# Performance work log

Hardware: AMD Instinct MI355X
Metric: run time of the kernel (lower is better)

The kernel has to match this reference:

```python
import jax, jax.numpy as jnp
import numpy as np

N = 10000
E = 160000
F_IN = 64
HID = 128
HEADS = 8
NC = 3
NEG_SLOPE = 0.2
EPS = 1e-16


def setup_inputs() -> dict:
    key = jax.random.key(0)
    ks = jax.random.split(key, 12)
    p = lambda k, shape: jax.random.normal(k, shape, jnp.float32) * 0.1
    return {
        "x": jax.random.normal(ks[0], (N, F_IN), jnp.float32),
        "edge_index": jax.random.randint(ks[1], (2, E), 0, N),
        # conv1: F_IN -> 8 heads x 128, concat -> 1024
        "W1": p(ks[2], (F_IN, HEADS * HID)),
        "a_src1": p(ks[3], (HEADS, HID)),
        "a_dst1": p(ks[4], (HEADS, HID)),
        "b1": jnp.zeros((HEADS * HID,), jnp.float32),
        # conv2: 1024 -> 8 heads x 64, concat -> 512
        "W2": p(ks[5], (HEADS * HID, HEADS * (HID // 2))),
        "a_src2": p(ks[6], (HEADS, HID // 2)),
        "a_dst2": p(ks[7], (HEADS, HID // 2)),
        "b2": jnp.zeros((HEADS * (HID // 2),), jnp.float32),
        # conv3: 512 -> 1 head x 3, mean (concat=False)
        "W3": p(ks[8], (HEADS * (HID // 2), NC)),
        "a_src3": p(ks[9], (1, NC)),
        "a_dst3": p(ks[10], (1, NC)),
        "b3": jnp.zeros((NC,), jnp.float32),
    }


def gat_conv(x, src, dst, W, a_src, a_dst, b, concat):
    """PyG-style GATConv (eval mode, self-loops already in src/dst)."""
    n = x.shape[0]
    H, C = a_src.shape
    h = (x @ W).reshape(n, H, C)                      # [N, H, C]
    s_src = jnp.sum(h * a_src[None], axis=-1)         # [N, H]
    s_dst = jnp.sum(h * a_dst[None], axis=-1)         # [N, H]
    e = jax.nn.leaky_relu(s_src[src] + s_dst[dst], NEG_SLOPE)  # [E, H]
    # segment softmax over incoming edges per destination node
    m = jax.ops.segment_max(e, dst, num_segments=n)   # [N, H]
    ex = jnp.exp(e - m[dst])
    denom = jax.ops.segment_sum(ex, dst, num_segments=n)
    alpha = ex / (denom[dst] + EPS)                   # [E, H]
    msg = h[src] * alpha[:, :, None]                  # [E, H, C]
    out = jax.ops.segment_sum(msg, dst, num_segments=n)  # [N, H, C]
    out = out.reshape(n, H * C) if concat else out.mean(axis=1)
    return out + b


def reference(x, edge_index, W1, a_src1, a_dst1, b1, W2, a_src2, a_dst2, b2, W3, a_src3, a_dst3, b3):
    n = x.shape[0]
    loop = jnp.arange(n, dtype=edge_index.dtype)
    src = jnp.concatenate([edge_index[0], loop])
    dst = jnp.concatenate([edge_index[1], loop])
    h = gat_conv(x, src, dst, W1, a_src1, a_dst1, b1, True)
    h = jax.nn.elu(h)
    h = gat_conv(h, src, dst, W2, a_src2, a_dst2, b2, True)
    h = jax.nn.elu(h)
    h = gat_conv(h, src, dst, W3, a_src3, a_dst3, b3, False)
    return jax.nn.log_softmax(h, axis=1)
```

## Files before the change

kernel.cpp:

```cpp
#include <hip/hip_runtime.h>
#include <math.h>

#define NEG_SLOPE 0.2f
#define EPS_DEN 1e-16f

typedef __attribute__((ext_vector_type(8))) short bf16x8;
typedef __attribute__((ext_vector_type(4))) float f32x4;

__device__ inline void split2(float a, short& hi, short& lo) {
    unsigned u = __float_as_uint(a);
    unsigned uh = (u + 0x8000u) & 0xFFFF0000u;
    float fh = __uint_as_float(uh);
    hi = (short)(uh >> 16);
    float r = a - fh;
    lo = (short)((__float_as_uint(r) + 0x8000u) >> 16);
}

__device__ inline unsigned short f2bf(float f) {
    unsigned u = __float_as_uint(f);
    return (unsigned short)((u + 0x7FFFu + ((u >> 16) & 1u)) >> 16);
}
__device__ inline float bflo(unsigned u) { return __uint_as_float(u << 16); }
__device__ inline float bfhi(unsigned u) { return __uint_as_float(u & 0xFFFF0000u); }

__global__ void k_count(const int* __restrict__ ei, int E, int Nn, int* counts) {
    int e = blockIdx.x * blockDim.x + threadIdx.x;
    int ET = E + Nn;
    if (e >= ET) return;
    int d = (e < E) ? ei[E + e] : (e - E);
    atomicAdd(&counts[d], 1);
}

__global__ void k_scan(const int* __restrict__ counts, int Nn, int ET, int* __restrict__ row_off) {
    __shared__ int lds[256];
    int t = threadIdx.x;
    int chunk = (Nn + 255) / 256;
    int b0 = t * chunk, b1 = min(Nn, b0 + chunk);
    int s = 0;
    for (int i = b0; i < b1; i++) s += counts[i];
    lds[t] = s;
    __syncthreads();
    #pragma unroll
    for (int d = 1; d < 256; d <<= 1) {
        int v = (t >= d) ? lds[t - d] : 0;
        __syncthreads();
        lds[t] += v;
        __syncthreads();
    }
    int run = (t == 0) ? 0 : lds[t - 1];
    for (int i = b0; i < b1; i++) { row_off[i] = run; run += counts[i]; }
    if (t == 0) row_off[Nn] = ET;
}

__global__ void k_scatter(const int* __restrict__ ei, int E, int Nn,
                          const int* __restrict__ row_off, int* cursor, int* __restrict__ col) {
    int e = blockIdx.x * blockDim.x + threadIdx.x;
    int ET = E + Nn;
    if (e >= ET) return;
    int d = (e < E) ? ei[E + e] : (e - E);
    int s = (e < E) ? ei[e] : (e - E);
    int pos = atomicAdd(&cursor[d], 1);
    col[row_off[d] + pos] = s;
}

__global__ void k_split_x(const float* __restrict__ x, short* __restrict__ A,
                          int M, int Mp, int K) {
    int i = blockIdx.x * blockDim.x + threadIdx.x;
    if (i >= Mp * K) return;
    int row = i / K, c = i - row * K;
    float v = (row < M) ? x[(size_t)row * K + c] : 0.f;
    short hi, lo;
    split2(v, hi, lo);
    A[(size_t)row * (2 * K) + c] = hi;
    A[(size_t)row * (2 * K) + K + c] = lo;
}

__global__ __launch_bounds__(256) void k_split_wt(const float* __restrict__ W,
                                                  short* __restrict__ Bt, int K, int N, int dup) {
    __shared__ float s[32][33];
    int k0 = blockIdx.x * 32, n0 = blockIdx.y * 32;
    int tx = threadIdx.x & 31, ty = threadIdx.x >> 5;
    for (int r = ty; r < 32; r += 8) s[r][tx] = W[(size_t)(k0 + r) * N + n0 + tx];
    __syncthreads();
    int ldbt = (1 + dup) * K;
    for (int r = ty; r < 32; r += 8) {
        float v = s[tx][r];
        unsigned u = __float_as_uint(v);
        short hi = (short)((u + 0x7FFFu + ((u >> 16) & 1u)) >> 16);
        size_t base = (size_t)(n0 + r) * ldbt + k0 + tx;
        Bt[base] = hi;
        if (dup) Bt[base + K] = hi;
    }
}

template<bool FUSESC>
__global__ __launch_bounds__(256) void k_mfma64(const short* __restrict__ A,
                                                const short* __restrict__ B,
                                                unsigned short* __restrict__ C,
                                                const float* __restrict__ a_src,
                                                const float* __restrict__ a_dst,
                                                float* __restrict__ ssrc,
                                                float* __restrict__ sdst,
                                                int M, int N, int Ktot,
                                                int lda, int ldb) {
    __shared__ short As[64 * 32];
    __shared__ short Bs[64 * 32];
    __shared__ float sred[4][64][2];
    int t = threadIdx.x;
    int lane = t & 63;
    int wid = t >> 6;

    int nbx = N >> 6;
    int nb = gridDim.x;
    int q = nb >> 3, r = nb & 7;
    int xcd = blockIdx.x & 7, pos = blockIdx.x >> 3;
    int L = (xcd < r ? xcd * (q + 1) : r * (q + 1) + (xcd - r) * q) + pos;
    int bn = (L % nbx) * 64;
    int bm = (L / nbx) * 64;

    int wm = (wid >> 1) * 32, wn = (wid & 1) * 32;
    int fr = lane & 15, kq = lane >> 4;

    int srow = t >> 2, sslot = t & 3;
    int sko = ((sslot ^ ((srow >> 1) & 3)) << 3);

    f32x4 acc[2][2] = {};

    for (int k0 = 0; k0 < Ktot; k0 += 32) {
        {
            const short* sa = A + (size_t)(bm + srow) * lda + k0 + sko;
            const short* sb = B + (size_t)(bn + srow) * ldb + k0 + sko;
            short* da = As + (size_t)(wid << 6) * 8;
            short* db = Bs + (size_t)(wid << 6) * 8;
            __builtin_amdgcn_global_load_lds((const __attribute__((address_space(1))) void*)sa,
                                             (__attribute__((address_space(3))) void*)da, 16, 0, 0);
            __builtin_amdgcn_global_load_lds((const __attribute__((address_space(1))) void*)sb,
                                             (__attribute__((address_space(3))) void*)db, 16, 0, 0);
        }
        __syncthreads();
        bf16x8 af[2], bfv[2];
        #pragma unroll
        for (int i = 0; i < 2; i++) {
            int rowa = wm + i * 16 + fr;
            int rowb = wn + i * 16 + fr;
            af[i]  = *(const bf16x8*)(As + rowa * 32 + ((kq ^ ((rowa >> 1) & 3)) << 3));
            bfv[i] = *(const bf16x8*)(Bs + rowb * 32 + ((kq ^ ((rowb >> 1) & 3)) << 3));
        }
        #pragma unroll
        for (int i = 0; i < 2; i++)
            #pragma unroll
            for (int j = 0; j < 2; j++)
                acc[i][j] = __builtin_amdgcn_mfma_f32_16x16x32_bf16(af[i], bfv[j], acc[i][j], 0, 0, 0);
        __syncthreads();
    }
    #pragma unroll
    for (int i = 0; i < 2; i++) {
        int rbase = bm + wm + i * 16 + kq * 4;
        #pragma unroll
        for (int j = 0; j < 2; j++) {
            int colc = bn + wn + j * 16 + fr;
            #pragma unroll
            for (int rg = 0; rg < 4; rg++) {
                int rr = rbase + rg;
                if (rr < M) C[(size_t)rr * N + colc] = f2bf(acc[i][j][rg]);
            }
        }
    }
    if (FUSESC) {
        float asv[2], adv[2];
        #pragma unroll
        for (int j = 0; j < 2; j++) {
            int colc = bn + wn + j * 16 + fr;
            asv[j] = a_src[colc];
            adv[j] = a_dst[colc];
        }
        float ps[8], pd[8];
        #pragma unroll
        for (int i = 0; i < 2; i++)
            #pragma unroll
            for (int rg = 0; rg < 4; rg++) {
                int k8 = i * 4 + rg;
                ps[k8] = acc[i][0][rg] * asv[0] + acc[i][1][rg] * asv[1];
                pd[k8] = acc[i][0][rg] * adv[0] + acc[i][1][rg] * adv[1];
            }
        #pragma unroll
        for (int k8 = 0; k8 < 8; k8++) {
            #pragma unroll
            for (int off = 1; off < 16; off <<= 1) {
                ps[k8] += __shfl_xor(ps[k8], off);
                pd[k8] += __shfl_xor(pd[k8], off);
            }
        }
        if (fr == 0) {
            #pragma unroll
            for (int i = 0; i < 2; i++)
                #pragma unroll
                for (int rg = 0; rg < 4; rg++) {
                    int rl = wm + i * 16 + kq * 4 + rg;
                    sred[wid][rl][0] = ps[i * 4 + rg];
                    sred[wid][rl][1] = pd[i * 4 + rg];
                }
        }
        __syncthreads();
        if ((wid & 1) == 0 && fr == 0) {
            int hh = bn >> 6;
            #pragma unroll
            for (int i = 0; i < 2; i++)
                #pragma unroll
                for (int rg = 0; rg < 4; rg++) {
                    int rl = wm + i * 16 + kq * 4 + rg;
                    int rr = bm + rl;
                    if (rr < M) {
                        ssrc[rr * 8 + hh] = sred[wid][rl][0] + sred[wid | 1][rl][0];
                        sdst[rr * 8 + hh] = sred[wid][rl][1] + sred[wid | 1][rl][1];
                    }
                }
        }
    }
}

template<int H, int C>
__global__ __launch_bounds__(256) void k_scores_bf(const unsigned short* __restrict__ h,
                                                   const float* __restrict__ a_src,
                                                   const float* __restrict__ a_dst,
                                                   float* __restrict__ ssrc,
                                                   float* __restrict__ sdst, int Nn) {
    constexpr int D = H * C;
    constexpr int PER = D / 64;
    constexpr int GRP = C / PER;
    int lane = threadIdx.x & 63;
    int n = blockIdx.x * 4 + (threadIdx.x >> 6);
    if (n >= Nn) return;
    const unsigned short* hp = h + (size_t)n * D + lane * PER;
    int cb = lane * PER;
    float as = 0.f, ad = 0.f;
    #pragma unroll
    for (int j0 = 0; j0 < PER; j0 += 8) {
        uint4 u = *(const uint4*)(hp + j0);
        int c = cb + j0;
        as += bflo(u.x) * a_src[c + 0] + bfhi(u.x) * a_src[c + 1]
            + bflo(u.y) * a_src[c + 2] + bfhi(u.y) * a_src[c + 3]
            + bflo(u.z) * a_src[c + 4] + bfhi(u.z) * a_src[c + 5]
            + bflo(u.w) * a_src[c + 6] + bfhi(u.w) * a_src[c + 7];
        ad += bflo(u.x) * a_dst[c + 0] + bfhi(u.x) * a_dst[c + 1]
            + bflo(u.y) * a_dst[c + 2] + bfhi(u.y) * a_dst[c + 3]
            + bflo(u.z) * a_dst[c + 4] + bfhi(u.z) * a_dst[c + 5]
            + bflo(u.w) * a_dst[c + 6] + bfhi(u.w) * a_dst[c + 7];
    }
    #pragma unroll
    for (int off = GRP >> 1; off >= 1; off >>= 1) {
        as += __shfl_xor(as, off);
        ad += __shfl_xor(ad, off);
    }
    if ((lane & (GRP - 1)) == 0) {
        int hh = lane / GRP;
        ssrc[n * H + hh] = as;
        sdst[n * H + hh] = ad;
    }
}

template<int H, int C, int CB, bool ELU, bool BFOUT>
__global__ __launch_bounds__(256) void k_agg_wave(const unsigned short* __restrict__ hsrc,
                                                  const float* __restrict__ ssrc,
                                                  const float* __restrict__ sdst,
                                                  const int* __restrict__ col,
                                                  const int* __restrict__ row_off,
                                                  const float* __restrict__ bias,
                                                  float* __restrict__ out,
                                                  unsigned short* __restrict__ osp,
                                                  int nw) {
    constexpr int D = H * C;
    int lane = threadIdx.x & 63;
    int w = blockIdx.x * 4 + (threadIdx.x >> 6);
    if (w >= nw) return;
    int n, cb;
    if (CB == 2) { n = w >> 1; cb = w & 1; } else { n = w; cb = 0; }
    int col0 = cb * 512 + lane * 8;
    int myhead = col0 / C;
    float sd = sdst[n * H + myhead];
    int beg = row_off[n], end = row_off[n + 1];
    const unsigned short* hbase = hsrc + col0;

    float acc[8] = {0.f, 0.f, 0.f, 0.f, 0.f, 0.f, 0.f, 0.f};
    float den = 0.f;
    #pragma unroll 2
    for (int j = beg; j < end; j++) {
        int cj = col[j];
        float s = ssrc[cj * H + myhead] + sd;
        s = (s >= 0.f) ? s : NEG_SLOPE * s;
        float ex = __expf(s);
        den += ex;
        uint4 u = *(const uint4*)(hbase + (size_t)cj * D);
        acc[0] += ex * bflo(u.x); acc[1] += ex * bfhi(u.x);
        acc[2] += ex * bflo(u.y); acc[3] += ex * bfhi(u.y);
        acc[4] += ex * bflo(u.z); acc[5] += ex * bfhi(u.z);
        acc[6] += ex * bflo(u.w); acc[7] += ex * bfhi(u.w);
    }
    float iv = 1.f / (den + EPS_DEN);
    float vals[8];
    #pragma unroll
    for (int v = 0; v < 8; v++) {
        float val = acc[v] * iv + bias[col0 + v];
        if (ELU) val = (val > 0.f) ? val : (__expf(val) - 1.f);
        vals[v] = val;
    }
    if (BFOUT) {
        uint4 o;
        o.x = (unsigned)f2bf(vals[0]) | ((unsigned)f2bf(vals[1]) << 16);
        o.y = (unsigned)f2bf(vals[2]) | ((unsigned)f2bf(vals[3]) << 16);
        o.z = (unsigned)f2bf(vals[4]) | ((unsigned)f2bf(vals[5]) << 16);
        o.w = (unsigned)f2bf(vals[6]) | ((unsigned)f2bf(vals[7]) << 16);
        *(uint4*)(osp + (size_t)n * D + col0) = o;
    } else {
        *(f32x4*)(out + (size_t)n * D + col0) = *(f32x4*)&vals[0];
        *(f32x4*)(out + (size_t)n * D + col0 + 4) = *(f32x4*)&vals[4];
    }
}

__global__ __launch_bounds__(256) void k_agg2_l3(const unsigned short* __restrict__ hsrc,
                                                 const float* __restrict__ ssrc,
                                                 const float* __restrict__ sdst,
                                                 const int* __restrict__ col,
                                                 const int* __restrict__ row_off,
                                                 const float* __restrict__ bias,
                                                 const float* __restrict__ W3,
                                                 const float* __restrict__ as3,
                                                 const float* __restrict__ ad3,
                                                 float* __restrict__ h3,
                                                 float* __restrict__ ssrc3,
                                                 float* __restrict__ sdst3,
                                                 int Nn) {
    constexpr int D = 512;
    int lane = threadIdx.x & 63;
    int n = blockIdx.x * 4 + (threadIdx.x >> 6);
    if (n >= Nn) return;
    int col0 = lane * 8;
    int myhead = lane >> 3;
    float sd = sdst[n * 8 + myhead];
    int beg = row_off[n], end = row_off[n + 1];
    const unsigned short* hbase = hsrc + col0;

    float acc[8] = {0.f, 0.f, 0.f, 0.f, 0.f, 0.f, 0.f, 0.f};
    float den = 0.f;
    #pragma unroll 2
    for (int j = beg; j < end; j++) {
        int cj = col[j];
        float s = ssrc[cj * 8 + myhead] + sd;
        s = (s >= 0.f) ? s : NEG_SLOPE * s;
        float ex = __expf(s);
        den += ex;
        uint4 u = *(const uint4*)(hbase + (size_t)cj * D);
        acc[0] += ex * bflo(u.x); acc[1] += ex * bfhi(u.x);
        acc[2] += ex * bflo(u.y); acc[3] += ex * bfhi(u.y);
        acc[4] += ex * bflo(u.z); acc[5] += ex * bfhi(u.z);
        acc[6] += ex * bflo(u.w); acc[7] += ex * bfhi(u.w);
    }
    float iv = 1.f / (den + EPS_DEN);
    float t0 = 0.f, t1 = 0.f, t2 = 0.f;
    #pragma unroll
    for (int v = 0; v < 8; v++) {
        float val = acc[v] * iv + bias[col0 + v];
        val = (val > 0.f) ? val : (__expf(val) - 1.f);
        const float* wp = W3 + (size_t)(col0 + v) * 3;
        t0 += val * wp[0];
        t1 += val * wp[1];
        t2 += val * wp[2];
    }
    #pragma unroll
    for (int off = 32; off >= 1; off >>= 1) {
        t0 += __shfl_xor(t0, off);
        t1 += __shfl_xor(t1, off);
        t2 += __shfl_xor(t2, off);
    }
    if (lane == 0) {
        h3[n * 3 + 0] = t0; h3[n * 3 + 1] = t1; h3[n * 3 + 2] = t2;
        ssrc3[n] = t0 * as3[0] + t1 * as3[1] + t2 * as3[2];
        sdst3[n] = t0 * ad3[0] + t1 * ad3[1] + t2 * ad3[2];
    }
}

__global__ void k_l3_fused(const float* __restrict__ h3, const float* __restrict__ ssrc,
                           const float* __restrict__ sdst, const int* __restrict__ col,
                           const int* __restrict__ row_off, const float* __restrict__ b3,
                           float* __restrict__ out, int Nn) {
    int n = blockIdx.x * blockDim.x + threadIdx.x;
    if (n >= Nn) return;
    int beg = row_off[n], end = row_off[n + 1];
    float sd = sdst[n];
    float den = 0.f, a0 = 0.f, a1 = 0.f, a2 = 0.f;
    for (int j = beg; j < end; j++) {
        int sI = col[j];
        float s = ssrc[sI] + sd;
        s = (s >= 0.f) ? s : NEG_SLOPE * s;
        float ex = __expf(s);
        den += ex;
        a0 += ex * h3[sI * 3 + 0];
        a1 += ex * h3[sI * 3 + 1];
        a2 += ex * h3[sI * 3 + 2];
    }
    float iv = 1.f / (den + EPS_DEN);
    float v0 = a0 * iv + b3[0], v1 = a1 * iv + b3[1], v2 = a2 * iv + b3[2];
    float m = fmaxf(v0, fmaxf(v1, v2));
    float l = logf(__expf(v0 - m) + __expf(v1 - m) + __expf(v2 - m));
    out[n * 3 + 0] = v0 - m - l;
    out[n * 3 + 1] = v1 - m - l;
    out[n * 3 + 2] = v2 - m - l;
}

extern "C" void kernel_launch(void* const* d_in, const int* in_sizes, int n_in,
                              void* d_out, int out_size, void* d_ws, size_t ws_size,
                              hipStream_t stream) {
    (void)n_in; (void)out_size; (void)ws_size;
    const float* x   = (const float*)d_in[0];
    const int*   ei  = (const int*)d_in[1];
    const float* W1  = (const float*)d_in[2];
    const float* as1 = (const float*)d_in[3];
    const float* ad1 = (const float*)d_in[4];
    const float* b1  = (const float*)d_in[5];
    const float* W2  = (const float*)d_in[6];
    const float* as2 = (const float*)d_in[7];
    const float* ad2 = (const float*)d_in[8];
    const float* b2  = (const float*)d_in[9];
    const float* W3  = (const float*)d_in[10];
    const float* as3 = (const float*)d_in[11];
    const float* ad3 = (const float*)d_in[12];
    const float* b3  = (const float*)d_in[13];
    float* out = (float*)d_out;

    const int Nn = in_sizes[0] / 64;
    const int E  = in_sizes[1] / 2;
    const int ET = E + Nn;
    const int Mp = ((Nn + 127) / 128) * 128;

    char* ws = (char*)d_ws;
    size_t off = 0;
    auto alloc = [&](size_t bytes) -> void* {
        void* p = ws + off;
        off = (off + bytes + 255) & ~(size_t)255;
        return p;
    };
    unsigned short* hbuf = (unsigned short*)alloc((size_t)Mp * 1024 * 2);
    unsigned short* A2   = (unsigned short*)alloc((size_t)Mp * 1024 * 2);
    float* h3   = (float*)alloc((size_t)Nn * 3 * 4);
    short* A1   = (short*)alloc((size_t)Mp * 128 * 2);
    short* B1t  = (short*)alloc((size_t)1024 * 128 * 2);
    short* B2t  = (short*)alloc((size_t)512 * 1024 * 2);
    float* ssrc = (float*)alloc((size_t)Nn * 8 * 4);
    float* sdst = (float*)alloc((size_t)Nn * 8 * 4);
    float* ssrcB= (float*)alloc((size_t)Nn * 8 * 4);
    float* sdstB= (float*)alloc((size_t)Nn * 8 * 4);
    float* ssrc3= (float*)alloc((size_t)Nn * 4);
    float* sdst3= (float*)alloc((size_t)Nn * 4);
    int* counts = (int*)alloc((size_t)Nn * 2 * 4);
    int* cursor = counts + Nn;
    int* row_off= (int*)alloc((size_t)(Nn + 1) * 4);
    int* colb   = (int*)alloc((size_t)ET * 4);

    hipMemsetAsync(counts, 0, (size_t)Nn * 2 * 4, stream);

    int etb = (ET + 255) / 256;
    k_count<<<etb, 256, 0, stream>>>(ei, E, Nn, counts);
    k_scan<<<1, 256, 0, stream>>>(counts, Nn, ET, row_off);
    k_scatter<<<etb, 256, 0, stream>>>(ei, E, Nn, row_off, cursor, colb);

    k_split_x<<<(Mp * 64 + 255) / 256, 256, 0, stream>>>(x, A1, Nn, Mp, 64);
    k_split_wt<<<dim3(64 / 32, 1024 / 32), 256, 0, stream>>>(W1, B1t, 64, 1024, 1);
    k_split_wt<<<dim3(1024 / 32, 512 / 32), 256, 0, stream>>>(W2, B2t, 1024, 512, 0);

    {
        int nb = (1024 / 64) * (Mp / 64);
        k_mfma64<false><<<nb, 256, 0, stream>>>(A1, B1t, hbuf, nullptr, nullptr, nullptr, nullptr,
                                                Nn, 1024, 128, 128, 128);
        k_scores_bf<8, 128><<<(Nn + 3) / 4, 256, 0, stream>>>(hbuf, as1, ad1, ssrc, sdst, Nn);
        int nw = Nn * 2;
        k_agg_wave<8, 128, 2, true, true><<<(nw + 3) / 4, 256, 0, stream>>>(
            hbuf, ssrc, sdst, colb, row_off, b1, nullptr, A2, nw);
    }
    {
        int nb = (512 / 64) * (Mp / 64);
        k_mfma64<true><<<nb, 256, 0, stream>>>((const short*)A2, B2t, hbuf, as2, ad2, ssrcB, sdstB,
                                               Nn, 512, 1024, 1024, 1024);
        k_agg2_l3<<<(Nn + 3) / 4, 256, 0, stream>>>(hbuf, ssrcB, sdstB, colb, row_off, b2,
                                                    W3, as3, ad3, h3, ssrc3, sdst3, Nn);
    }
    k_l3_fused<<<(Nn + 255) / 256, 256, 0, stream>>>(h3, ssrc3, sdst3, colb, row_off, b3, out, Nn);
}
```

Before: 190.3 us.

## Merge preprocessing kernels and fuse layer-1 attention scores into a wider GEMM

The separate count, x-split and two weight-split kernels are folded into one k_pre launch that routes blocks to each task by block index. For layer 1, a new GEMM kernel with 64x128 tiles covers one full head per block and computes the src/dst attention scores in its epilogue, so the standalone k_scores_bf pass that re-read the 1024-wide bf16 hidden buffer is removed. This saves several launches and one full read of the layer-1 features, at the cost of more accumulator registers in the wider tile and a more complex block-routing kernel.

Measured after the change: 182.3 us. -4.2%, faster.

```diff
diff --git a/kernel.cpp b/kernel.cpp
--- a/kernel.cpp
+++ b/kernel.cpp
@@ -23,63 +23,50 @@
 __device__ inline float bflo(unsigned u) { return __uint_as_float(u << 16); }
 __device__ inline float bfhi(unsigned u) { return __uint_as_float(u & 0xFFFF0000u); }
 
-__global__ void k_count(const int* __restrict__ ei, int E, int Nn, int* counts) {
-    int e = blockIdx.x * blockDim.x + threadIdx.x;
+__global__ __launch_bounds__(256) void k_pre(const int* __restrict__ ei, int E, int Nn,
+                                             int* __restrict__ counts,
+                                             const float* __restrict__ x, short* __restrict__ A1, int Mp,
+                                             const float* __restrict__ W1, short* __restrict__ B1t,
+                                             const float* __restrict__ W2, short* __restrict__ B2t) {
+    __shared__ float s[32][33];
+    int t = threadIdx.x;
+    int b = blockIdx.x;
     int ET = E + Nn;
-    if (e >= ET) return;
-    int d = (e < E) ? ei[E + e] : (e - E);
-    atomicAdd(&counts[d], 1);
-}
-
-__global__ void k_scan(const int* __restrict__ counts, int Nn, int ET, int* __restrict__ row_off) {
-    __shared__ int lds[256];
-    int t = threadIdx.x;
-    int chunk = (Nn + 255) / 256;
-    int b0 = t * chunk, b1 = min(Nn, b0 + chunk);
-    int s = 0;
-    for (int i = b0; i < b1; i++) s += counts[i];
-    lds[t] = s;
-    __syncthreads();
-    #pragma unroll
-    for (int d = 1; d < 256; d <<= 1) {
-        int v = (t >= d) ? lds[t - d] : 0;
-        __syncthreads();
-        lds[t] += v;
-        __syncthreads();
-    }
-    int run = (t == 0) ? 0 : lds[t - 1];
-    for (int i = b0; i < b1; i++) { row_off[i] = run; run += counts[i]; }
-    if (t == 0) row_off[Nn] = ET;
-}
-
-__global__ void k_scatter(const int* __restrict__ ei, int E, int Nn,
-                          const int* __restrict__ row_off, int* cursor, int* __restrict__ col) {
-    int e = blockIdx.x * blockDim.x + threadIdx.x;
-    int ET = E + Nn;
-    if (e >= ET) return;
-    int d = (e < E) ? ei[E + e] : (e - E);
-    int s = (e < E) ? ei[e] : (e - E);
-    int pos = atomicAdd(&cursor[d], 1);
-    col[row_off[d] + pos] = s;
-}
-
-__global__ void k_split_x(const float* __restrict__ x, short* __restrict__ A,
-                          int M, int Mp, int K) {
-    int i = blockIdx.x * blockDim.x + threadIdx.x;
-    if (i >= Mp * K) return;
-    int row = i / K, c = i - row * K;
-    float v = (row < M) ? x[(size_t)row * K + c] : 0.f;
-    short hi, lo;
-    split2(v, hi, lo);
-    A[(size_t)row * (2 * K) + c] = hi;
-    A[(size_t)row * (2 * K) + K + c] = lo;
-}
-
-__global__ __launch_bounds__(256) void k_split_wt(const float* __restrict__ W,
-                                                  short* __restrict__ Bt, int K, int N, int dup) {
-    __shared__ float s[32][33];
-    int k0 = blockIdx.x * 32, n0 = blockIdx.y * 32;
-    int tx = threadIdx.x & 31, ty = threadIdx.x >> 5;
+    int etb = (ET + 255) / 256;
+    int xb = (Mp * 64 + 255) / 256;
+    if (b < etb) {
+        int e = b * 256 + t;
+        if (e < ET) {
+            int d = (e < E) ? ei[E + e] : (e - E);
+            atomicAdd(&counts[d], 1);
+        }
+        return;
+    }
+    b -= etb;
+    if (b < xb) {
+        int i = b * 256 + t;
+        if (i < Mp * 64) {
+            int row = i >> 6, c = i & 63;
+            float v = (row < Nn) ? x[(size_t)row * 64 + c] : 0.f;
+            short hi, lo;
+            split2(v, hi, lo);
+            A1[(size_t)row * 128 + c] = hi;
+            A1[(size_t)row * 128 + 64 + c] = lo;
+        }
+        return;
+    }
+    b -= xb;
+    const float* W; short* Bt; int K, N, dup, kb, nb;
+    if (b < 64) {
+        W = W1; Bt = B1t; K = 64; N = 1024; dup = 1;
+        kb = b & 1; nb = b >> 1;
+    } else {
+        b -= 64;
+        W = W2; Bt = B2t; K = 1024; N = 512; dup = 0;
+        kb = b & 31; nb = b >> 5;
+    }
+    int k0 = kb * 32, n0 = nb * 32;
+    int tx = t & 31, ty = t >> 5;
     for (int r = ty; r < 32; r += 8) s[r][tx] = W[(size_t)(k0 + r) * N + n0 + tx];
     __syncthreads();
     int ldbt = (1 + dup) * K;
@@ -93,7 +80,172 @@
     }
 }
 
-template<bool FUSESC>
+__global__ void k_scan(const int* __restrict__ counts, int Nn, int ET, int* __restrict__ row_off) {
+    __shared__ int lds[256];
+    int t = threadIdx.x;
+    int chunk = (Nn + 255) / 256;
+    int b0 = t * chunk, b1 = min(Nn, b0 + chunk);
+    int s = 0;
+    for (int i = b0; i < b1; i++) s += counts[i];
+    lds[t] = s;
+    __syncthreads();
+    #pragma unroll
+    for (int d = 1; d < 256; d <<= 1) {
+        int v = (t >= d) ? lds[t - d] : 0;
+        __syncthreads();
+        lds[t] += v;
+        __syncthreads();
+    }
+    int run = (t == 0) ? 0 : lds[t - 1];
+    for (int i = b0; i < b1; i++) { row_off[i] = run; run += counts[i]; }
+    if (t == 0) row_off[Nn] = ET;
+}
+
+__global__ void k_scatter(const int* __restrict__ ei, int E, int Nn,
+                          const int* __restrict__ row_off, int* cursor, int* __restrict__ col) {
+    int e = blockIdx.x * blockDim.x + threadIdx.x;
+    int ET = E + Nn;
+    if (e >= ET) return;
+    int d = (e < E) ? ei[E + e] : (e - E);
+    int s = (e < E) ? ei[e] : (e - E);
+    int pos = atomicAdd(&cursor[d], 1);
+    col[row_off[d] + pos] = s;
+}
+
+__global__ __launch_bounds__(256) void k_mfma_w(const short* __restrict__ A,
+                                                const short* __restrict__ B,
+                                                unsigned short* __restrict__ C,
+                                                const float* __restrict__ a_src,
+                                                const float* __restrict__ a_dst,
+                                                float* __restrict__ ssrc,
+                                                float* __restrict__ sdst,
+                                                int M, int N, int Ktot,
+                                                int lda, int ldb) {
+    __shared__ short As[64 * 32];
+    __shared__ short Bs[128 * 32];
+    __shared__ float sred[4][64][2];
+    int t = threadIdx.x;
+    int lane = t & 63;
+    int wid = t >> 6;
+
+    int nbx = N >> 7;
+    int nb = gridDim.x;
+    int q = nb >> 3, r = nb & 7;
+    int xcd = blockIdx.x & 7, pos = blockIdx.x >> 3;
+    int L = (xcd < r ? xcd * (q + 1) : r * (q + 1) + (xcd - r) * q) + pos;
+    int bn = (L % nbx) * 128;
+    int bm = (L / nbx) * 64;
+
+    int wm = (wid & 1) * 32, wn = (wid >> 1) * 64;
+    int fr = lane & 15, kq = lane >> 4;
+
+    int srow = t >> 2, sslot = t & 3;
+    int sko = ((sslot ^ ((srow >> 1) & 3)) << 3);
+
+    f32x4 acc[2][4] = {};
+
+    for (int k0 = 0; k0 < Ktot; k0 += 32) {
+        {
+            const short* sa = A + (size_t)(bm + srow) * lda + k0 + sko;
+            short* da = As + (size_t)(wid << 6) * 8;
+            __builtin_amdgcn_global_load_lds((const __attribute__((address_space(1))) void*)sa,
+                                             (__attribute__((address_space(3))) void*)da, 16, 0, 0);
+            #pragma unroll
+            for (int qq = 0; qq < 2; qq++) {
+                int v = qq * 256 + t;
+                int rowb = v >> 2, slotb = v & 3;
+                int skob = ((slotb ^ ((rowb >> 1) & 3)) << 3);
+                const short* sb = B + (size_t)(bn + rowb) * ldb + k0 + skob;
+                short* db = Bs + (size_t)(qq * 256 + (wid << 6)) * 8;
+                __builtin_amdgcn_global_load_lds((const __attribute__((address_space(1))) void*)sb,
+                                                 (__attribute__((address_space(3))) void*)db, 16, 0, 0);
+            }
+        }
+        __syncthreads();
+        bf16x8 af[2], bfv[4];
+        #pragma unroll
+        for (int i = 0; i < 2; i++) {
+            int rowa = wm + i * 16 + fr;
+            af[i] = *(const bf16x8*)(As + rowa * 32 + ((kq ^ ((rowa >> 1) & 3)) << 3));
+        }
+        #pragma unroll
+        for (int j = 0; j < 4; j++) {
+            int rowb = wn + j * 16 + fr;
+            bfv[j] = *(const bf16x8*)(Bs + rowb * 32 + ((kq ^ ((rowb >> 1) & 3)) << 3));
+        }
+        #pragma unroll
+        for (int i = 0; i < 2; i++)
+            #pragma unroll
+            for (int j = 0; j < 4; j++)
+                acc[i][j] = __builtin_amdgcn_mfma_f32_16x16x32_bf16(af[i], bfv[j], acc[i][j], 0, 0, 0);
+        __syncthreads();
+    }
+    #pragma unroll
+    for (int i = 0; i < 2; i++) {
+        int rbase = bm + wm + i * 16 + kq * 4;
+        #pragma unroll
+        for (int j = 0; j < 4; j++) {
+            int colc = bn + wn + j * 16 + fr;
+            #pragma unroll
+            for (int rg = 0; rg < 4; rg++) {
+                int rr = rbase + rg;
+                if (rr < M) C[(size_t)rr * N + colc] = f2bf(acc[i][j][rg]);
+            }
+        }
+    }
+    float asv[4], adv[4];
+    #pragma unroll
+    for (int j = 0; j < 4; j++) {
+        int colc = bn + wn + j * 16 + fr;
+        asv[j] = a_src[colc];
+        adv[j] = a_dst[colc];
+    }
+    float ps[8], pd[8];
+    #pragma unroll
+    for (int i = 0; i < 2; i++)
+        #pragma unroll
+        for (int rg = 0; rg < 4; rg++) {
+            int k8 = i * 4 + rg;
+            ps[k8] = acc[i][0][rg] * asv[0] + acc[i][1][rg] * asv[1]
+                   + acc[i][2][rg] * asv[2] + acc[i][3][rg] * asv[3];
+            pd[k8] = acc[i][0][rg] * adv[0] + acc[i][1][rg] * adv[1]
+                   + acc[i][2][rg] * adv[2] + acc[i][3][rg] * adv[3];
+        }
+    #pragma unroll
+    for (int k8 = 0; k8 < 8; k8++) {
+        #pragma unroll
+        for (int off = 1; off < 16; off <<= 1) {
+            ps[k8] += __shfl_xor(ps[k8], off);
+            pd[k8] += __shfl_xor(pd[k8], off);
+        }
+    }
+    if (fr == 0) {
+        #pragma unroll
+        for (int i = 0; i < 2; i++)
+            #pragma unroll
+            for (int rg = 0; rg < 4; rg++) {
+                int rl = wm + i * 16 + kq * 4 + rg;
+                sred[wid][rl][0] = ps[i * 4 + rg];
+                sred[wid][rl][1] = pd[i * 4 + rg];
+            }
+    }
+    __syncthreads();
+    if (wid < 2 && fr == 0) {
+        int hh = bn >> 7;
+        #pragma unroll
+        for (int i = 0; i < 2; i++)
+            #pragma unroll
+            for (int rg = 0; rg < 4; rg++) {
+                int rl = wm + i * 16 + kq * 4 + rg;
+                int rr = bm + rl;
+                if (rr < M) {
+                    ssrc[rr * 8 + hh] = sred[wid][rl][0] + sred[wid + 2][rl][0];
+                    sdst[rr * 8 + hh] = sred[wid][rl][1] + sred[wid + 2][rl][1];
+                }
+            }
+    }
+}
+
 __global__ __launch_bounds__(256) void k_mfma64(const short* __restrict__ A,
                                                 const short* __restrict__ B,
                                                 unsigned short* __restrict__ C,
@@ -166,96 +318,54 @@
             }
         }
     }
-    if (FUSESC) {
-        float asv[2], adv[2];
-        #pragma unroll
-        for (int j = 0; j < 2; j++) {
-            int colc = bn + wn + j * 16 + fr;
-            asv[j] = a_src[colc];
-            adv[j] = a_dst[colc];
-        }
-        float ps[8], pd[8];
+    float asv[2], adv[2];
+    #pragma unroll
+    for (int j = 0; j < 2; j++) {
+        int colc = bn + wn + j * 16 + fr;
+        asv[j] = a_src[colc];
+        adv[j] = a_dst[colc];
+    }
+    float ps[8], pd[8];
+    #pragma unroll
+    for (int i = 0; i < 2; i++)
+        #pragma unroll
+        for (int rg = 0; rg < 4; rg++) {
+            int k8 = i * 4 + rg;
+            ps[k8] = acc[i][0][rg] * asv[0] + acc[i][1][rg] * asv[1];
+            pd[k8] = acc[i][0][rg] * adv[0] + acc[i][1][rg] * adv[1];
+        }
+    #pragma unroll
+    for (int k8 = 0; k8 < 8; k8++) {
+        #pragma unroll
+        for (int off = 1; off < 16; off <<= 1) {
+            ps[k8] += __shfl_xor(ps[k8], off);
+            pd[k8] += __shfl_xor(pd[k8], off);
+        }
+    }
+    if (fr == 0) {
         #pragma unroll
         for (int i = 0; i < 2; i++)
             #pragma unroll
             for (int rg = 0; rg < 4; rg++) {
-                int k8 = i * 4 + rg;
-                ps[k8] = acc[i][0][rg] * asv[0] + acc[i][1][rg] * asv[1];
-                pd[k8] = acc[i][0][rg] * adv[0] + acc[i][1][rg] * adv[1];
-            }
-        #pragma unroll
-        for (int k8 = 0; k8 < 8; k8++) {
-            #pragma unroll
-            for (int off = 1; off < 16; off <<= 1) {
-                ps[k8] += __shfl_xor(ps[k8], off);
-                pd[k8] += __shfl_xor(pd[k8], off);
-            }
-        }
-        if (fr == 0) {
-            #pragma unroll
-            for (int i = 0; i < 2; i++)
-                #pragma unroll
-                for (int rg = 0; rg < 4; rg++) {
-                    int rl = wm + i * 16 + kq * 4 + rg;
-                    sred[wid][rl][0] = ps[i * 4 + rg];
-                    sred[wid][rl][1] = pd[i * 4 + rg];
+                int rl = wm + i * 16 + kq * 4 + rg;
+                sred[wid][rl][0] = ps[i * 4 + rg];
+                sred[wid][rl][1] = pd[i * 4 + rg];
+            }
+    }
+    __syncthreads();
+    if ((wid & 1) == 0 && fr == 0) {
+        int hh = bn >> 6;
+        #pragma unroll
+        for (int i = 0; i < 2; i++)
+            #pragma unroll
+            for (int rg = 0; rg < 4; rg++) {
+                int rl = wm + i * 16 + kq * 4 + rg;
+                int rr = bm + rl;
+                if (rr < M) {
+                    ssrc[rr * 8 + hh] = sred[wid][rl][0] + sred[wid | 1][rl][0];
+                    sdst[rr * 8 + hh] = sred[wid][rl][1] + sred[wid | 1][rl][1];
                 }
-        }
-        __syncthreads();
-        if ((wid & 1) == 0 && fr == 0) {
-            int hh = bn >> 6;
-            #pragma unroll
-            for (int i = 0; i < 2; i++)
-                #pragma unroll
-                for (int rg = 0; rg < 4; rg++) {
-                    int rl = wm + i * 16 + kq * 4 + rg;
-                    int rr = bm + rl;
-                    if (rr < M) {
-                        ssrc[rr * 8 + hh] = sred[wid][rl][0] + sred[wid | 1][rl][0];
-                        sdst[rr * 8 + hh] = sred[wid][rl][1] + sred[wid | 1][rl][1];
-                    }
-                }
-        }
-    }
-}
-
-template<int H, int C>
-__global__ __launch_bounds__(256) void k_scores_bf(const unsigned short* __restrict__ h,
-                                                   const float* __restrict__ a_src,
-                                                   const float* __restrict__ a_dst,
-                                                   float* __restrict__ ssrc,
-                                                   float* __restrict__ sdst, int Nn) {
-    constexpr int D = H * C;
-    constexpr int PER = D / 64;
-    constexpr int GRP = C / PER;
-    int lane = threadIdx.x & 63;
-    int n = blockIdx.x * 4 + (threadIdx.x >> 6);
-    if (n >= Nn) return;
-    const unsigned short* hp = h + (size_t)n * D + lane * PER;
-    int cb = lane * PER;
-    float as = 0.f, ad = 0.f;
-    #pragma unroll
-    for (int j0 = 0; j0 < PER; j0 += 8) {
-        uint4 u = *(const uint4*)(hp + j0);
-        int c = cb + j0;
-        as += bflo(u.x) * a_src[c + 0] + bfhi(u.x) * a_src[c + 1]
-            + bflo(u.y) * a_src[c + 2] + bfhi(u.y) * a_src[c + 3]
-            + bflo(u.z) * a_src[c + 4] + bfhi(u.z) * a_src[c + 5]
-            + bflo(u.w) * a_src[c + 6] + bfhi(u.w) * a_src[c + 7];
-        ad += bflo(u.x) * a_dst[c + 0] + bfhi(u.x) * a_dst[c + 1]
-            + bflo(u.y) * a_dst[c + 2] + bfhi(u.y) * a_dst[c + 3]
-            + bflo(u.z) * a_dst[c + 4] + bfhi(u.z) * a_dst[c + 5]
-            + bflo(u.w) * a_dst[c + 6] + bfhi(u.w) * a_dst[c + 7];
-    }
-    #pragma unroll
-    for (int off = GRP >> 1; off >= 1; off >>= 1) {
-        as += __shfl_xor(as, off);
-        ad += __shfl_xor(ad, off);
-    }
-    if ((lane & (GRP - 1)) == 0) {
-        int hh = lane / GRP;
-        ssrc[n * H + hh] = as;
-        sdst[n * H + hh] = ad;
+            }
     }
 }
 
@@ -459,27 +569,24 @@
     hipMemsetAsync(counts, 0, (size_t)Nn * 2 * 4, stream);
 
     int etb = (ET + 255) / 256;
-    k_count<<<etb, 256, 0, stream>>>(ei, E, Nn, counts);
+    int xb = (Mp * 64 + 255) / 256;
+    int preb = etb + xb + 64 + 512;
+    k_pre<<<preb, 256, 0, stream>>>(ei, E, Nn, counts, x, A1, Mp, W1, B1t, W2, B2t);
     k_scan<<<1, 256, 0, stream>>>(counts, Nn, ET, row_off);
     k_scatter<<<etb, 256, 0, stream>>>(ei, E, Nn, row_off, cursor, colb);
 
-    k_split_x<<<(Mp * 64 + 255) / 256, 256, 0, stream>>>(x, A1, Nn, Mp, 64);
-    k_split_wt<<<dim3(64 / 32, 1024 / 32), 256, 0, stream>>>(W1, B1t, 64, 1024, 1);
-    k_split_wt<<<dim3(1024 / 32, 512 / 32), 256, 0, stream>>>(W2, B2t, 1024, 512, 0);
-
     {
-        int nb = (1024 / 64) * (Mp / 64);
-        k_mfma64<false><<<nb, 256, 0, stream>>>(A1, B1t, hbuf, nullptr, nullptr, nullptr, nullptr,
-                                                Nn, 1024, 128, 128, 128);
-        k_scores_bf<8, 128><<<(Nn + 3) / 4, 256, 0, stream>>>(hbuf, as1, ad1, ssrc, sdst, Nn);
+        int nb = (1024 / 128) * (Mp / 64);
+        k_mfma_w<<<nb, 256, 0, stream>>>(A1, B1t, hbuf, as1, ad1, ssrc, sdst,
+                                         Nn, 1024, 128, 128, 128);
         int nw = Nn * 2;
         k_agg_wave<8, 128, 2, true, true><<<(nw + 3) / 4, 256, 0, stream>>>(
             hbuf, ssrc, sdst, colb, row_off, b1, nullptr, A2, nw);
     }
     {
         int nb = (512 / 64) * (Mp / 64);
-        k_mfma64<true><<<nb, 256, 0, stream>>>((const short*)A2, B2t, hbuf, as2, ad2, ssrcB, sdstB,
-                                               Nn, 512, 1024, 1024, 1024);
+        k_mfma64<<<nb, 256, 0, stream>>>((const short*)A2, B2t, hbuf, as2, ad2, ssrcB, sdstB,
+                                         Nn, 512, 1024, 1024, 1024);
         k_agg2_l3<<<(Nn + 3) / 4, 256, 0, stream>>>(hbuf, ssrcB, sdstB, colb, row_off, b2,
                                                     W3, as3, ad3, h3, ssrc3, sdst3, Nn);
     }
```
